# Kernel tuning notes

Hardware: AMD Instinct MI355X
Metric: run time of the kernel (lower is better)

The kernel has to match this reference:

```python
import jax, jax.numpy as jnp
import numpy as np

NUM_HEADS = 16
EMBED = 1024
HEAD_DIM = EMBED // NUM_HEADS


def setup_inputs() -> dict:
    key = jax.random.key(0)
    k1, k2, k3, k4, k5 = jax.random.split(key, 5)
    B, N, D = 16, 1024, EMBED
    s_in = 1.0 / np.sqrt(D)
    x = jax.random.normal(k1, (B, N, D), dtype=jnp.float32)
    # Linear weights stored as [in, out] so y = x @ W + b (equiv to torch x @ W.T + b)
    W_qkv = jax.random.uniform(k2, (D, 3 * D), dtype=jnp.float32, minval=-s_in, maxval=s_in)
    b_qkv = jax.random.uniform(k3, (3 * D,), dtype=jnp.float32, minval=-s_in, maxval=s_in)
    W_fc = jax.random.uniform(k4, (D, D), dtype=jnp.float32, minval=-s_in, maxval=s_in)
    b_fc = jax.random.uniform(k5, (D,), dtype=jnp.float32, minval=-s_in, maxval=s_in)
    return {"x": x, "W_qkv": W_qkv, "b_qkv": b_qkv, "W_fc": W_fc, "b_fc": b_fc}


def reference(x, W_qkv, b_qkv, W_fc, b_fc):
    B, N, D = x.shape
    H, d_k = NUM_HEADS, HEAD_DIM
    qkv = x @ W_qkv + b_qkv                      # [B, N, 3D]
    qkv = qkv.reshape(B, N, 3, H, d_k)
    qkv = jnp.transpose(qkv, (2, 0, 3, 1, 4))    # [3, B, H, N, d_k]
    Q, K, V = qkv[0], qkv[1], qkv[2]
    scale = 1.0 / jnp.sqrt(jnp.asarray(d_k, dtype=x.dtype))
    scores = jnp.einsum("bhqd,bhkd->bhqk", Q, K) * scale
    attn = jax.nn.softmax(scores, axis=-1)       # dropout is identity in eval mode
    context = jnp.einsum("bhqk,bhkd->bhqd", attn, V)
    context = jnp.transpose(context, (0, 2, 1, 3)).reshape(B, N, D)
    return context @ W_fc + b_fc
```

## Files before the change

### kernel.cpp

```cpp
#include <hip/hip_runtime.h>
#include <cstdint>
#include <cstddef>

typedef unsigned short u16;
typedef __bf16 bf16_t;
typedef bf16_t bf16x8 __attribute__((ext_vector_type(8)));
typedef float f32x4 __attribute__((ext_vector_type(4)));

#define MFMA16(a, b, c) __builtin_amdgcn_mfma_f32_16x16x32_bf16((a), (b), (c), 0, 0, 0)
#define GLOBAL_AS __attribute__((address_space(1)))
#define LDS_AS __attribute__((address_space(3)))

#define SOFT_M 8.0f

__device__ __forceinline__ u16 f2bf(float f) {
    unsigned u = __float_as_uint(f);
    u += 0x7FFFu + ((u >> 16) & 1u);
    return (u16)(u >> 16);
}
__device__ __forceinline__ u16 f2bf_trunc(float f) {
    return (u16)(__float_as_uint(f) >> 16);
}
__device__ __forceinline__ void gll16(const u16* g, u16* l) {
    __builtin_amdgcn_global_load_lds((const GLOBAL_AS unsigned int*)g,
                                     (LDS_AS unsigned int*)l, 16, 0, 0);
}

__global__ __launch_bounds__(256) void conv_x_kernel(const float* __restrict__ x,
                                                     u16* __restrict__ xb) {
    int i = blockIdx.x * 256 + threadIdx.x;
    float4 v = ((const float4*)x)[i];
    ushort4 o;
    o.x = f2bf(v.x); o.y = f2bf(v.y); o.z = f2bf(v.z); o.w = f2bf(v.w);
    ((ushort4*)xb)[i] = o;
}

__global__ __launch_bounds__(256) void transpose_w_kernel(const float* __restrict__ W,
                                                          u16* __restrict__ Wt,
                                                          int R, int C) {
    __shared__ u16 tile[32][33];
    int c0 = blockIdx.x * 32, r0 = blockIdx.y * 32;
    int tx = threadIdx.x, ty = threadIdx.y;
#pragma unroll
    for (int i = 0; i < 4; i++)
        tile[ty + i * 8][tx] = f2bf(W[(size_t)(r0 + ty + i * 8) * C + c0 + tx]);
    __syncthreads();
#pragma unroll
    for (int i = 0; i < 4; i++)
        Wt[(size_t)(c0 + ty + i * 8) * R + r0 + tx] = tile[tx][ty + i * 8];
}

__global__ __launch_bounds__(256) void gemm_qkv_kernel(const u16* __restrict__ A,
                                                       const u16* __restrict__ Bt,
                                                       const float* __restrict__ bias,
                                                       u16* __restrict__ Qb,
                                                       u16* __restrict__ Kb,
                                                       u16* __restrict__ Vt) {
    const int K = 1024;
    __shared__ u16 As[128 * 32];
    __shared__ u16 Bs[128 * 32];
    int t = threadIdx.x;
    int m0 = blockIdx.x * 128, n0 = blockIdx.y * 128;
    int lane = t & 63, wid = t >> 6;
    int lr = lane & 15, quad = lane >> 4;
    int wm = (wid >> 1) * 64, wn = (wid & 1) * 64;
    int srow = lane >> 2, scol = (lane & 3) * 8;

    f32x4 acc[4][4];
    f32x4 zf = {0.f, 0.f, 0.f, 0.f};
#pragma unroll
    for (int i = 0; i < 4; i++)
#pragma unroll
        for (int j = 0; j < 4; j++) acc[i][j] = zf;

    for (int k0 = 0; k0 < K; k0 += 32) {
        __syncthreads();
#pragma unroll
        for (int i = 0; i < 2; i++) {
            int c = wid * 2 + i;
            int row = c * 16 + srow;
            gll16(A + (size_t)(m0 + row) * K + k0 + scol, &As[c * 512]);
            gll16(Bt + (size_t)(n0 + row) * K + k0 + scol, &Bs[c * 512]);
        }
        __syncthreads();
        bf16x8 af[4], bfr[4];
#pragma unroll
        for (int mt = 0; mt < 4; mt++)
            af[mt] = *(const bf16x8*)&As[(wm + mt * 16 + lr) * 32 + quad * 8];
#pragma unroll
        for (int nt = 0; nt < 4; nt++)
            bfr[nt] = *(const bf16x8*)&Bs[(wn + nt * 16 + lr) * 32 + quad * 8];
#pragma unroll
        for (int mt = 0; mt < 4; mt++)
#pragma unroll
            for (int nt = 0; nt < 4; nt++)
                acc[mt][nt] = MFMA16(af[mt], bfr[nt], acc[mt][nt]);
    }

    int s = n0 >> 10;
    if (s == 2) {
#pragma unroll
        for (int nt = 0; nt < 4; nt++) {
            int col = n0 + wn + nt * 16 + lr;
            int h = (col >> 6) & 15, d = col & 63;
            float bv = bias[col];
#pragma unroll
            for (int mt = 0; mt < 4; mt++) {
                f32x4 v = acc[mt][nt];
                int mb = m0 + wm + mt * 16 + quad * 4;
                int bb = mb >> 10, nn = mb & 1023;
                ushort4 o;
                o.x = f2bf(v[0] + bv); o.y = f2bf(v[1] + bv);
                o.z = f2bf(v[2] + bv); o.w = f2bf(v[3] + bv);
                *(ushort4*)&Vt[(((size_t)(bb * 16 + h)) * 64 + d) * 1024 + nn] = o;
            }
        }
    } else {
        u16* dst = (s == 0) ? Qb : Kb;
        float scale = (s == 0) ? 0.125f * 1.44269504089f : 1.0f;
#pragma unroll
        for (int nt = 0; nt < 4; nt++) {
            int col = n0 + wn + nt * 16 + lr;
            int h = (col >> 6) & 15, d = col & 63;
            float bv = bias[col];
#pragma unroll
            for (int mt = 0; mt < 4; mt++) {
                f32x4 v = acc[mt][nt];
#pragma unroll
                for (int r = 0; r < 4; r++) {
                    int m = m0 + wm + mt * 16 + quad * 4 + r;
                    int bb = m >> 10, nn = m & 1023;
                    dst[(((size_t)(bb * 16 + h)) * 1024 + nn) * 64 + d] =
                        f2bf((v[r] + bv) * scale);
                }
            }
        }
    }
}

__global__ __launch_bounds__(256, 3) void flash_attn_kernel(const u16* __restrict__ Qb,
                                                            const u16* __restrict__ Kb,
                                                            const u16* __restrict__ Vt,
                                                            u16* __restrict__ ctx) {
    __shared__ u16 Ks[2][64 * 72];
    __shared__ u16 Vs[2][64 * 72];
    __shared__ u16 Hs[16 * 72];
    __shared__ u16 Ps[4][16 * 72];
    int t = threadIdx.x, lane = t & 63, wid = t >> 6;
    int lr = lane & 15, quad = lane >> 4;
    int bh = blockIdx.x, q0 = blockIdx.y * 128;
    int b = bh >> 4, h = bh & 15;

    for (int idx = t; idx < 16 * 72; idx += 256) {
        int r = idx / 72;
        Hs[idx] = (r == 0) ? 0x3F80 : 0;
    }

    const u16* Kg = Kb + (size_t)bh * 65536;
    const u16* Vg = Vt + (size_t)bh * 65536;
    int srow = t >> 3, scg = (t & 7) * 8;

    uint4 kr[2], vr[2];
#pragma unroll
    for (int i = 0; i < 2; i++) {
        int row = srow + i * 32;
        kr[i] = *(const uint4*)(Kg + (size_t)row * 64 + scg);
        vr[i] = *(const uint4*)(Vg + (size_t)row * 1024 + scg);
    }

    const u16* Qw = Qb + ((size_t)bh * 1024 + q0 + wid * 32) * 64;
    bf16x8 qf[2][2];
#pragma unroll
    for (int mt = 0; mt < 2; mt++)
#pragma unroll
        for (int kk = 0; kk < 2; kk++)
            qf[mt][kk] = *(const bf16x8*)(Qw + (mt * 16 + lr) * 64 + kk * 32 + quad * 8);

#pragma unroll
    for (int i = 0; i < 2; i++) {
        int row = srow + i * 32;
        *(uint4*)&Ks[0][row * 72 + scg] = kr[i];
        *(uint4*)&Vs[0][row * 72 + scg] = vr[i];
    }
    __syncthreads();

    bf16x8 of[2];
#pragma unroll
    for (int kc = 0; kc < 2; kc++)
        of[kc] = *(const bf16x8*)&Hs[lr * 72 + kc * 32 + quad * 8];

    f32x4 oacc[2][4], lacc[2];
    f32x4 zf = {0.f, 0.f, 0.f, 0.f};
#pragma unroll
    for (int mt = 0; mt < 2; mt++) {
#pragma unroll
        for (int dt = 0; dt < 4; dt++) oacc[mt][dt] = zf;
        lacc[mt] = zf;
    }
    u16* Pw = Ps[wid];

    for (int kt = 0; kt < 16; kt++) {
        int cur = kt & 1;
        if (kt < 15) {
#pragma unroll
            for (int i = 0; i < 2; i++) {
                int row = srow + i * 32;
                kr[i] = *(const uint4*)(Kg + (size_t)((kt + 1) * 64 + row) * 64 + scg);
                vr[i] = *(const uint4*)(Vg + (size_t)row * 1024 + (kt + 1) * 64 + scg);
            }
        }
        if (kt > 0) __syncthreads();

        f32x4 sc[2][4];
#pragma unroll
        for (int mt = 0; mt < 2; mt++)
#pragma unroll
            for (int nt = 0; nt < 4; nt++) sc[mt][nt] = zf;
#pragma unroll
        for (int nt = 0; nt < 4; nt++) {
            bf16x8 kf0 = *(const bf16x8*)&Ks[cur][(nt * 16 + lr) * 72 + quad * 8];
            bf16x8 kf1 = *(const bf16x8*)&Ks[cur][(nt * 16 + lr) * 72 + 32 + quad * 8];
#pragma unroll
            for (int mt = 0; mt < 2; mt++) {
                sc[mt][nt] = MFMA16(qf[mt][0], kf0, sc[mt][nt]);
                sc[mt][nt] = MFMA16(qf[mt][1], kf1, sc[mt][nt]);
            }
        }

#pragma unroll
        for (int mt = 0; mt < 2; mt++) {
#pragma unroll
            for (int nt = 0; nt < 4; nt++)
#pragma unroll
                for (int r = 0; r < 4; r++) {
                    float p = __builtin_amdgcn_exp2f(sc[mt][nt][r] - SOFT_M);
                    Pw[(quad * 4 + r) * 72 + nt * 16 + lr] = f2bf_trunc(p);
                }
#pragma unroll
            for (int kc = 0; kc < 2; kc++) {
                bf16x8 pa = *(const bf16x8*)&Pw[lr * 72 + kc * 32 + quad * 8];
#pragma unroll
                for (int dt = 0; dt < 4; dt++) {
                    bf16x8 vv = *(const bf16x8*)&Vs[cur][(dt * 16 + lr) * 72 + kc * 32 + quad * 8];
                    oacc[mt][dt] = MFMA16(pa, vv, oacc[mt][dt]);
                }
                lacc[mt] = MFMA16(pa, of[kc], lacc[mt]);
            }
        }

        if (kt < 15) {
            int nxt = cur ^ 1;
#pragma unroll
            for (int i = 0; i < 2; i++) {
                int row = srow + i * 32;
                *(uint4*)&Ks[nxt][row * 72 + scg] = kr[i];
                *(uint4*)&Vs[nxt][row * 72 + scg] = vr[i];
            }
        }
    }

#pragma unroll
    for (int mt = 0; mt < 2; mt++) {
        float inv[4];
#pragma unroll
        for (int r = 0; r < 4; r++) {
            float l = __shfl(lacc[mt][r], lane & 48);
            inv[r] = 1.0f / l;
        }
#pragma unroll
        for (int dt = 0; dt < 4; dt++)
#pragma unroll
            for (int r = 0; r < 4; r++) {
                int row = q0 + wid * 32 + mt * 16 + quad * 4 + r;
                int d = dt * 16 + lr;
                ctx[((size_t)b * 1024 + row) * 1024 + h * 64 + d] = f2bf(oacc[mt][dt][r] * inv[r]);
            }
    }
}

__global__ __launch_bounds__(256) void gemm_proj_kernel(const u16* __restrict__ A,
                                                        const u16* __restrict__ Bt,
                                                        const float* __restrict__ bias,
                                                        float* __restrict__ out) {
    const int K = 1024;
    __shared__ u16 As[128 * 32];
    __shared__ u16 Bs[128 * 32];
    int t = threadIdx.x;
    int m0 = blockIdx.x * 128, n0 = blockIdx.y * 128;
    int lane = t & 63, wid = t >> 6;
    int lr = lane & 15, quad = lane >> 4;
    int wm = (wid >> 1) * 64, wn = (wid & 1) * 64;
    int srow = lane >> 2, scol = (lane & 3) * 8;

    f32x4 acc[4][4];
    f32x4 zf = {0.f, 0.f, 0.f, 0.f};
#pragma unroll
    for (int i = 0; i < 4; i++)
#pragma unroll
        for (int j = 0; j < 4; j++) acc[i][j] = zf;

    for (int k0 = 0; k0 < K; k0 += 32) {
        __syncthreads();
#pragma unroll
        for (int i = 0; i < 2; i++) {
            int c = wid * 2 + i;
            int row = c * 16 + srow;
            gll16(A + (size_t)(m0 + row) * K + k0 + scol, &As[c * 512]);
            gll16(Bt + (size_t)(n0 + row) * K + k0 + scol, &Bs[c * 512]);
        }
        __syncthreads();
        bf16x8 af[4], bfr[4];
#pragma unroll
        for (int mt = 0; mt < 4; mt++)
            af[mt] = *(const bf16x8*)&As[(wm + mt * 16 + lr) * 32 + quad * 8];
#pragma unroll
        for (int nt = 0; nt < 4; nt++)
            bfr[nt] = *(const bf16x8*)&Bs[(wn + nt * 16 + lr) * 32 + quad * 8];
#pragma unroll
        for (int mt = 0; mt < 4; mt++)
#pragma unroll
            for (int nt = 0; nt < 4; nt++)
                acc[mt][nt] = MFMA16(af[mt], bfr[nt], acc[mt][nt]);
    }

#pragma unroll
    for (int nt = 0; nt < 4; nt++) {
        int col = n0 + wn + nt * 16 + lr;
        float bv = bias[col];
#pragma unroll
        for (int mt = 0; mt < 4; mt++) {
            f32x4 v = acc[mt][nt];
#pragma unroll
            for (int r = 0; r < 4; r++) {
                int m = m0 + wm + mt * 16 + quad * 4 + r;
                out[(size_t)m * 1024 + col] = v[r] + bv;
            }
        }
    }
}

extern "C" void kernel_launch(void* const* d_in, const int* in_sizes, int n_in,
                              void* d_out, int out_size, void* d_ws, size_t ws_size,
                              hipStream_t stream) {
    const float* x     = (const float*)d_in[0];
    const float* W_qkv = (const float*)d_in[1];
    const float* b_qkv = (const float*)d_in[2];
    const float* W_fc  = (const float*)d_in[3];
    const float* b_fc  = (const float*)d_in[4];
    float* out = (float*)d_out;
    char* ws = (char*)d_ws;

    u16* xb  = (u16*)(ws + 0);
    u16* wqt = (u16*)(ws + 33554432);
    u16* wft = (u16*)(ws + 39845888);
    u16* Qb  = (u16*)(ws + 41943040);
    u16* Kb  = (u16*)(ws + 75497472);
    u16* Vt  = (u16*)(ws + 109051904);
    u16* ctx = (u16*)(ws + 0);

    conv_x_kernel<<<16384, 256, 0, stream>>>(x, xb);
    transpose_w_kernel<<<dim3(96, 32), dim3(32, 8), 0, stream>>>(W_qkv, wqt, 1024, 3072);
    transpose_w_kernel<<<dim3(32, 32), dim3(32, 8), 0, stream>>>(W_fc, wft, 1024, 1024);
    gemm_qkv_kernel<<<dim3(128, 24), 256, 0, stream>>>(xb, wqt, b_qkv, Qb, Kb, Vt);
    flash_attn_kernel<<<dim3(256, 8), 256, 0, stream>>>(Qb, Kb, Vt, ctx);
    gemm_proj_kernel<<<dim3(128, 8), 256, 0, stream>>>(ctx, wft, b_fc, out);
}
```

Before: 489.2 us.

## Keep softmax probabilities in registers via transposed QK^T and lane shuffles

Swaps the operand order of the QK^T MFMA so each lane holds a column-oriented score tile, then builds the PV A-operand directly in registers using xor-16 shuffles instead of writing P to LDS and reading it back. The row-sum MFMA against a ones vector is replaced by scalar per-lane accumulation reduced with shuffles at the end, and the V read offset is permuted to match the new key ordering. Removing the Ps/Hs shared buffers frees LDS, and the occupancy hint is raised from 3 to 4 blocks per CU. The risks are register pressure at the higher occupancy target and subtle ordering bugs in the lane permutation.

```diff
diff --git a/kernel.cpp b/kernel.cpp
--- a/kernel.cpp
+++ b/kernel.cpp
@@ -138,24 +138,47 @@
     }
 }
 
-__global__ __launch_bounds__(256, 3) void flash_attn_kernel(const u16* __restrict__ Qb,
+__device__ __forceinline__ uint4 build_pa(f32x4 s0, f32x4 s1, float& lacc, bool qodd) {
+    unsigned w[4];
+    float part = 0.f;
+#pragma unroll
+    for (int half = 0; half < 2; half++) {
+        unsigned lo = f2bf_trunc(__builtin_amdgcn_exp2f(s0[half * 2] - SOFT_M));
+        unsigned hi = f2bf_trunc(__builtin_amdgcn_exp2f(s0[half * 2 + 1] - SOFT_M));
+        part += __uint_as_float(lo << 16) + __uint_as_float(hi << 16);
+        w[half] = lo | (hi << 16);
+    }
+#pragma unroll
+    for (int half = 0; half < 2; half++) {
+        unsigned lo = f2bf_trunc(__builtin_amdgcn_exp2f(s1[half * 2] - SOFT_M));
+        unsigned hi = f2bf_trunc(__builtin_amdgcn_exp2f(s1[half * 2 + 1] - SOFT_M));
+        part += __uint_as_float(lo << 16) + __uint_as_float(hi << 16);
+        w[2 + half] = lo | (hi << 16);
+    }
+    lacc += part;
+    unsigned x0 = qodd ? w[0] : w[2];
+    unsigned x1 = qodd ? w[1] : w[3];
+    unsigned y0 = __shfl_xor(x0, 16);
+    unsigned y1 = __shfl_xor(x1, 16);
+    uint4 r;
+    r.x = qodd ? y0 : w[0];
+    r.y = qodd ? y1 : w[1];
+    r.z = qodd ? w[2] : y0;
+    r.w = qodd ? w[3] : y1;
+    return r;
+}
+
+__global__ __launch_bounds__(256, 4) void flash_attn_kernel(const u16* __restrict__ Qb,
                                                             const u16* __restrict__ Kb,
                                                             const u16* __restrict__ Vt,
                                                             u16* __restrict__ ctx) {
     __shared__ u16 Ks[2][64 * 72];
     __shared__ u16 Vs[2][64 * 72];
-    __shared__ u16 Hs[16 * 72];
-    __shared__ u16 Ps[4][16 * 72];
     int t = threadIdx.x, lane = t & 63, wid = t >> 6;
     int lr = lane & 15, quad = lane >> 4;
     int bh = blockIdx.x, q0 = blockIdx.y * 128;
     int b = bh >> 4, h = bh & 15;
 
-    for (int idx = t; idx < 16 * 72; idx += 256) {
-        int r = idx / 72;
-        Hs[idx] = (r == 0) ? 0x3F80 : 0;
-    }
-
     const u16* Kg = Kb + (size_t)bh * 65536;
     const u16* Vg = Vt + (size_t)bh * 65536;
     int srow = t >> 3, scg = (t & 7) * 8;
@@ -184,20 +207,15 @@
     }
     __syncthreads();
 
-    bf16x8 of[2];
-#pragma unroll
-    for (int kc = 0; kc < 2; kc++)
-        of[kc] = *(const bf16x8*)&Hs[lr * 72 + kc * 32 + quad * 8];
-
-    f32x4 oacc[2][4], lacc[2];
+    f32x4 oacc[2][4];
     f32x4 zf = {0.f, 0.f, 0.f, 0.f};
 #pragma unroll
-    for (int mt = 0; mt < 2; mt++) {
+    for (int mt = 0; mt < 2; mt++)
 #pragma unroll
         for (int dt = 0; dt < 4; dt++) oacc[mt][dt] = zf;
-        lacc[mt] = zf;
-    }
-    u16* Pw = Ps[wid];
+    float lsum0 = 0.f, lsum1 = 0.f;
+    bool qodd = (quad & 1) != 0;
+    int vperm8 = (((quad & 1) << 1) | (quad >> 1)) * 8;
 
     for (int kt = 0; kt < 16; kt++) {
         int cur = kt & 1;
@@ -222,29 +240,22 @@
             bf16x8 kf1 = *(const bf16x8*)&Ks[cur][(nt * 16 + lr) * 72 + 32 + quad * 8];
 #pragma unroll
             for (int mt = 0; mt < 2; mt++) {
-                sc[mt][nt] = MFMA16(qf[mt][0], kf0, sc[mt][nt]);
-                sc[mt][nt] = MFMA16(qf[mt][1], kf1, sc[mt][nt]);
-            }
-        }
-
-#pragma unroll
-        for (int mt = 0; mt < 2; mt++) {
-#pragma unroll
-            for (int nt = 0; nt < 4; nt++)
-#pragma unroll
-                for (int r = 0; r < 4; r++) {
-                    float p = __builtin_amdgcn_exp2f(sc[mt][nt][r] - SOFT_M);
-                    Pw[(quad * 4 + r) * 72 + nt * 16 + lr] = f2bf_trunc(p);
-                }
-#pragma unroll
-            for (int kc = 0; kc < 2; kc++) {
-                bf16x8 pa = *(const bf16x8*)&Pw[lr * 72 + kc * 32 + quad * 8];
-#pragma unroll
-                for (int dt = 0; dt < 4; dt++) {
-                    bf16x8 vv = *(const bf16x8*)&Vs[cur][(dt * 16 + lr) * 72 + kc * 32 + quad * 8];
-                    oacc[mt][dt] = MFMA16(pa, vv, oacc[mt][dt]);
-                }
-                lacc[mt] = MFMA16(pa, of[kc], lacc[mt]);
+                sc[mt][nt] = MFMA16(kf0, qf[mt][0], sc[mt][nt]);
+                sc[mt][nt] = MFMA16(kf1, qf[mt][1], sc[mt][nt]);
+            }
+        }
+
+#pragma unroll
+        for (int kc = 0; kc < 2; kc++) {
+            uint4 pw0 = build_pa(sc[0][kc * 2], sc[0][kc * 2 + 1], lsum0, qodd);
+            uint4 pw1 = build_pa(sc[1][kc * 2], sc[1][kc * 2 + 1], lsum1, qodd);
+            bf16x8 pa0 = *(const bf16x8*)&pw0;
+            bf16x8 pa1 = *(const bf16x8*)&pw1;
+#pragma unroll
+            for (int dt = 0; dt < 4; dt++) {
+                bf16x8 vv = *(const bf16x8*)&Vs[cur][(dt * 16 + lr) * 72 + kc * 32 + vperm8];
+                oacc[0][dt] = MFMA16(pa0, vv, oacc[0][dt]);
+                oacc[1][dt] = MFMA16(pa1, vv, oacc[1][dt]);
             }
         }
 
@@ -261,20 +272,21 @@
 
 #pragma unroll
     for (int mt = 0; mt < 2; mt++) {
-        float inv[4];
+        float lf = (mt == 0) ? lsum0 : lsum1;
+        lf += __shfl_xor(lf, 16);
+        lf += __shfl_xor(lf, 32);
+        float inv = 1.0f / lf;
 #pragma unroll
         for (int r = 0; r < 4; r++) {
-            float l = __shfl(lacc[mt][r], lane & 48);
-            inv[r] = 1.0f / l;
-        }
-#pragma unroll
-        for (int dt = 0; dt < 4; dt++)
-#pragma unroll
-            for (int r = 0; r < 4; r++) {
-                int row = q0 + wid * 32 + mt * 16 + quad * 4 + r;
+            float invr = __shfl(inv, (lane & 48) | (quad * 4 + r));
+            int row = q0 + wid * 32 + mt * 16 + quad * 4 + r;
+#pragma unroll
+            for (int dt = 0; dt < 4; dt++) {
                 int d = dt * 16 + lr;
-                ctx[((size_t)b * 1024 + row) * 1024 + h * 64 + d] = f2bf(oacc[mt][dt][r] * inv[r]);
-            }
+                ctx[((size_t)b * 1024 + row) * 1024 + h * 64 + d] =
+                    f2bf(oacc[mt][dt][r] * invr);
+            }
+        }
     }
 }
 
```

After: 503.2 us. 2.9% more time.
